# Kernel optimization log

Hardware: AMD Instinct MI355X
Metric: run time of the kernel (lower is better)

## Reference

```python
import jax, jax.numpy as jnp
import numpy as np

EMBED_DIM = 1024
NUM_HEADS = 16
HEAD_DIM = EMBED_DIM // NUM_HEADS

def setup_inputs() -> dict:
    key = jax.random.key(0)
    k1, k2, k3 = jax.random.split(key, 3)
    x = jax.random.normal(k1, (4, 2048, EMBED_DIM), dtype=jnp.float32)
    # Linear weights stored as [out, in] like torch; we apply x @ W.T
    W_qkv = jax.random.normal(k2, (3 * EMBED_DIM, EMBED_DIM), dtype=jnp.float32) * (EMBED_DIM ** -0.5)
    W_proj = jax.random.normal(k3, (EMBED_DIM, EMBED_DIM), dtype=jnp.float32) * (EMBED_DIM ** -0.5)
    return {"x": x, "W_qkv": W_qkv, "W_proj": W_proj}

def reference(x, W_qkv, W_proj):
    B, T, C = x.shape
    H, D = NUM_HEADS, HEAD_DIM
    qkv = x @ W_qkv.T                          # [B,T,3C]
    q, k, v = jnp.split(qkv, 3, axis=-1)
    q = q.reshape(B, T, H, D).transpose(0, 2, 1, 3)  # [B,H,T,D]
    k = k.reshape(B, T, H, D).transpose(0, 2, 1, 3)
    v = v.reshape(B, T, H, D).transpose(0, 2, 1, 3)
    scores = jnp.einsum('bhqd,bhkd->bhqk', q, k) / jnp.sqrt(jnp.asarray(D, x.dtype))
    causal = jnp.tril(jnp.ones((T, T), dtype=bool))
    scores = jnp.where(causal, scores, -jnp.inf)
    weights = jax.nn.softmax(scores, axis=-1)
    out = jnp.einsum('bhqk,bhkd->bhqd', weights, v)  # [B,H,T,D]
    out = out.transpose(0, 2, 1, 3).reshape(B, T, C)
    return out @ W_proj.T
```

## Files before the change

### kernel.cpp

```cpp
#include <hip/hip_runtime.h>

#define T_SEQ 2048
#define NB 4
#define NH 16
#define HD 64
#define CDIM 1024
#define MROWS (NB * T_SEQ)

typedef __attribute__((ext_vector_type(8))) short short8;
typedef __attribute__((ext_vector_type(4))) float floatx4;

static __device__ __forceinline__ unsigned short f2bf(float f) {
  union { float f; unsigned int i; } c; c.f = f;
  return (unsigned short)((c.i + 0x7FFFu + ((c.i >> 16) & 1u)) >> 16);
}
static __device__ __forceinline__ unsigned short f2bf_trunc(float f) {
  union { float f; unsigned int i; } c; c.f = f;
  return (unsigned short)(c.i >> 16);
}

static __device__ __forceinline__ void gl2lds16(const void* g, void* l) {
  __builtin_amdgcn_global_load_lds(
      (const __attribute__((address_space(1))) unsigned int*)g,
      (__attribute__((address_space(3))) unsigned int*)l, 16, 0, 0);
}

#define X4 (MROWS * CDIM / 4)
#define WQ4 (3 * CDIM * CDIM / 4)
#define WP4 (CDIM * CDIM / 4)
__global__ __launch_bounds__(256) void cast3_bf16(const float* __restrict__ x,
                                                  const float* __restrict__ wq,
                                                  const float* __restrict__ wp,
                                                  unsigned short* __restrict__ out) {
  const int i = blockIdx.x * 256 + threadIdx.x;
  const float* src; int off;
  if (i < X4) { src = x; off = i; }
  else if (i < X4 + WQ4) { src = wq; off = i - X4; }
  else { src = wp; off = i - X4 - WQ4; }
  const float4 v = ((const float4*)src)[off];
  ushort4 o;
  o.x = f2bf(v.x); o.y = f2bf(v.y); o.z = f2bf(v.z); o.w = f2bf(v.w);
  ((ushort4*)out)[i] = o;
}

#define Q_PRESCALE 0.18033688f

__global__ __launch_bounds__(256) void gemm_bf16_qkv(
    const unsigned short* __restrict__ A,
    const unsigned short* __restrict__ B,
    unsigned short* __restrict__ Oq,
    unsigned short* __restrict__ Ok,
    unsigned short* __restrict__ Ovt,
    const int K)
{
  __shared__ unsigned short As[2][128 * 32];
  __shared__ unsigned short Bs[2][128 * 32];
  const int tid = threadIdx.x;
  const int w = tid >> 6, l = tid & 63;
  const int quad = l >> 4, l15 = l & 15;
  const int m0 = blockIdx.y * 128, n0 = blockIdx.x * 128;
  const int wm = (w >> 1) * 64, wn = (w & 1) * 64;
  const int srow = l >> 2;
  const int scol = ((l & 3) ^ (srow & 3)) * 8;

  floatx4 acc[4][4];
#pragma unroll
  for (int mi = 0; mi < 4; ++mi)
#pragma unroll
    for (int ni = 0; ni < 4; ++ni) acc[mi][ni] = (floatx4){0.f, 0.f, 0.f, 0.f};

  const unsigned short* Ag = A + (size_t)(m0 + w * 32 + srow) * K + scol;
  const unsigned short* Bg = B + (size_t)(n0 + w * 32 + srow) * K + scol;
  const int d0 = (w * 32) * 32, d1 = (w * 32 + 16) * 32;
  const int sq = quad ^ (l15 & 3);

  gl2lds16(Ag, &As[0][d0]);
  gl2lds16(Ag + (size_t)16 * K, &As[0][d1]);
  gl2lds16(Bg, &Bs[0][d0]);
  gl2lds16(Bg + (size_t)16 * K, &Bs[0][d1]);

  for (int k0 = 0; k0 < K; k0 += 32) {
    const int cur = (k0 >> 5) & 1, nxt = 1 - cur;
    __syncthreads();
    if (k0 + 32 < K) {
      gl2lds16(Ag + k0 + 32, &As[nxt][d0]);
      gl2lds16(Ag + (size_t)16 * K + k0 + 32, &As[nxt][d1]);
      gl2lds16(Bg + k0 + 32, &Bs[nxt][d0]);
      gl2lds16(Bg + (size_t)16 * K + k0 + 32, &Bs[nxt][d1]);
    }
    short8 af[4], bfr[4];
#pragma unroll
    for (int mi = 0; mi < 4; ++mi)
      af[mi] = *(const short8*)&As[cur][(wm + mi * 16 + l15) * 32 + sq * 8];
#pragma unroll
    for (int ni = 0; ni < 4; ++ni)
      bfr[ni] = *(const short8*)&Bs[cur][(wn + ni * 16 + l15) * 32 + sq * 8];
#pragma unroll
    for (int mi = 0; mi < 4; ++mi)
#pragma unroll
      for (int ni = 0; ni < 4; ++ni)
        acc[mi][ni] = __builtin_amdgcn_mfma_f32_16x16x32_bf16(bfr[ni], af[mi], acc[mi][ni], 0, 0, 0);
  }

  const int which = n0 >> 10;
  if (which < 2) {
    unsigned short* dst = (which == 0) ? Oq : Ok;
    const float sc = (which == 0) ? Q_PRESCALE : 1.0f;
#pragma unroll
    for (int ni = 0; ni < 4; ++ni) {
      const int n = n0 + wn + ni * 16 + quad * 4;
      const int h = (n >> 6) & (NH - 1), d = n & (HD - 1);
#pragma unroll
      for (int mi = 0; mi < 4; ++mi) {
        const int m = m0 + wm + mi * 16 + l15;
        const int b = m >> 11, t = m & (T_SEQ - 1);
        ushort4 pk;
        pk.x = f2bf(acc[mi][ni][0] * sc); pk.y = f2bf(acc[mi][ni][1] * sc);
        pk.z = f2bf(acc[mi][ni][2] * sc); pk.w = f2bf(acc[mi][ni][3] * sc);
        *(ushort4*)(dst + (((size_t)(b * NH + h) * T_SEQ + t) << 6) + d) = pk;
      }
    }
  } else {
#pragma unroll
    for (int ni = 0; ni < 4; ++ni) {
      const int nb = n0 + wn + ni * 16 + quad * 4;
      const int h = (nb >> 6) & (NH - 1);
#pragma unroll
      for (int mi = 0; mi < 4; ++mi) {
        const int m = m0 + wm + mi * 16 + l15;
        const int b = m >> 11, t = m & (T_SEQ - 1);
#pragma unroll
        for (int r = 0; r < 4; ++r) {
          const int d = (nb + r) & (HD - 1);
          Ovt[((size_t)((b * NH + h) * HD + d) << 11) + t] = f2bf(acc[mi][ni][r]);
        }
      }
    }
  }
}

__global__ __launch_bounds__(256) void gemm_bf16_proj(
    const unsigned short* __restrict__ A,
    const unsigned short* __restrict__ B,
    float* __restrict__ O,
    const int N, const int K)
{
  __shared__ unsigned short As[2][128 * 32];
  __shared__ unsigned short Bs[2][128 * 32];
  const int tid = threadIdx.x;
  const int w = tid >> 6, l = tid & 63;
  const int quad = l >> 4, l15 = l & 15;
  const int m0 = blockIdx.y * 128, n0 = blockIdx.x * 128;
  const int wm = (w >> 1) * 64, wn = (w & 1) * 64;
  const int srow = l >> 2;
  const int scol = ((l & 3) ^ (srow & 3)) * 8;

  floatx4 acc[4][4];
#pragma unroll
  for (int mi = 0; mi < 4; ++mi)
#pragma unroll
    for (int ni = 0; ni < 4; ++ni) acc[mi][ni] = (floatx4){0.f, 0.f, 0.f, 0.f};

  const unsigned short* Ag = A + (size_t)(m0 + w * 32 + srow) * K + scol;
  const unsigned short* Bg = B + (size_t)(n0 + w * 32 + srow) * K + scol;
  const int d0 = (w * 32) * 32, d1 = (w * 32 + 16) * 32;
  const int sq = quad ^ (l15 & 3);

  gl2lds16(Ag, &As[0][d0]);
  gl2lds16(Ag + (size_t)16 * K, &As[0][d1]);
  gl2lds16(Bg, &Bs[0][d0]);
  gl2lds16(Bg + (size_t)16 * K, &Bs[0][d1]);

  for (int k0 = 0; k0 < K; k0 += 32) {
    const int cur = (k0 >> 5) & 1, nxt = 1 - cur;
    __syncthreads();
    if (k0 + 32 < K) {
      gl2lds16(Ag + k0 + 32, &As[nxt][d0]);
      gl2lds16(Ag + (size_t)16 * K + k0 + 32, &As[nxt][d1]);
      gl2lds16(Bg + k0 + 32, &Bs[nxt][d0]);
      gl2lds16(Bg + (size_t)16 * K + k0 + 32, &Bs[nxt][d1]);
    }
    short8 af[4], bfr[4];
#pragma unroll
    for (int mi = 0; mi < 4; ++mi)
      af[mi] = *(const short8*)&As[cur][(wm + mi * 16 + l15) * 32 + sq * 8];
#pragma unroll
    for (int ni = 0; ni < 4; ++ni)
      bfr[ni] = *(const short8*)&Bs[cur][(wn + ni * 16 + l15) * 32 + sq * 8];
#pragma unroll
    for (int mi = 0; mi < 4; ++mi)
#pragma unroll
      for (int ni = 0; ni < 4; ++ni)
        acc[mi][ni] = __builtin_amdgcn_mfma_f32_16x16x32_bf16(bfr[ni], af[mi], acc[mi][ni], 0, 0, 0);
  }

#pragma unroll
  for (int ni = 0; ni < 4; ++ni) {
    const int n = n0 + wn + ni * 16 + quad * 4;
#pragma unroll
    for (int mi = 0; mi < 4; ++mi) {
      const int m = m0 + wm + mi * 16 + l15;
      *(float4*)(O + (size_t)m * N + n) =
          make_float4(acc[mi][ni][0], acc[mi][ni][1], acc[mi][ni][2], acc[mi][ni][3]);
    }
  }
}

#define TK 64
#define PTP 72

__global__ __launch_bounds__(512) void attn_mfma(
    const unsigned short* __restrict__ Q,
    const unsigned short* __restrict__ K,
    const unsigned short* __restrict__ Vt,
    unsigned short* __restrict__ O)
{
  __shared__ unsigned short Ks[2][TK * HD];
  __shared__ unsigned short Vts[2][HD * TK];
  __shared__ unsigned short Pt[8][16 * PTP];
  const int tid = threadIdx.x;
  const int w = tid >> 6, l = tid & 63;
  const int quad = l >> 4, l15 = l & 15;
  const int drow = 8 * w + (l >> 3);
  const int dch = ((l & 7) ^ (l >> 3)) * 8;
  const int sw7 = l15 & 7;

  const int bh = blockIdx.x & 63;
  const int pp = blockIdx.x >> 6;
  const int b = bh >> 4, h = bh & 15;
  const size_t hoff = (size_t)bh * T_SEQ * HD;
  const unsigned short* Qh = Q + hoff;
  const unsigned short* Kdma = K + hoff + (size_t)drow * HD + dch;
  const unsigned short* Vdma = Vt + hoff + ((size_t)drow << 11) + dch;
  const int wb = w * 512;

  short8 ones;
#pragma unroll
  for (int j = 0; j < 8; ++j) ones[j] = (short)0x3F80;

#pragma unroll 1
  for (int ii = 0; ii < 2; ++ii) {
    const int qtile = ii ? pp : (15 - pp);
    const int qw = qtile * 128 + w * 16;

    short8 qf[2];
    {
      const int qrow = qw + l15;
      qf[0] = *(const short8*)(Qh + (size_t)qrow * HD + quad * 8);
      qf[1] = *(const short8*)(Qh + (size_t)qrow * HD + 32 + quad * 8);
    }

    floatx4 Of[4];
#pragma unroll
    for (int dc = 0; dc < 4; ++dc) Of[dc] = (floatx4){0.f, 0.f, 0.f, 0.f};
    floatx4 lacc = (floatx4){0.f, 0.f, 0.f, 0.f};

    const int nkt = 2 * qtile + 2;
    __syncthreads();
    gl2lds16(Kdma, &Ks[0][wb]);
    gl2lds16(Vdma, &Vts[0][wb]);

    for (int kt = 0; kt < nkt; ++kt) {
      const int kt0 = kt * TK;
      const int cur = kt & 1, nxt = 1 - cur;
      __syncthreads();
      if (kt + 1 < nkt) {
        gl2lds16(Kdma + (size_t)(kt0 + TK) * HD, &Ks[nxt][wb]);
        gl2lds16(Vdma + kt0 + TK, &Vts[nxt][wb]);
      }

      if (qw + 15 >= kt0) {
        floatx4 Sf[4];
#pragma unroll
        for (int cb = 0; cb < 4; ++cb) {
          Sf[cb] = (floatx4){0.f, 0.f, 0.f, 0.f};
          const int krow = cb * 16 + l15;
#pragma unroll
          for (int h2 = 0; h2 < 2; ++h2) {
            const int ch = (h2 * 4 + quad) ^ sw7;
            const short8 kf = *(const short8*)&Ks[cur][krow * 64 + ch * 8];
            Sf[cb] = __builtin_amdgcn_mfma_f32_16x16x32_bf16(kf, qf[h2], Sf[cb], 0, 0, 0);
          }
        }
        const bool full = (kt0 + 63 <= qw);
        const int q = qw + l15;
#pragma unroll
        for (int cb = 0; cb < 4; ++cb) {
          const int key0 = kt0 + cb * 16 + quad * 4;
          ushort4 pk;
          if (full) {
            pk.x = f2bf_trunc(exp2f(Sf[cb][0]));
            pk.y = f2bf_trunc(exp2f(Sf[cb][1]));
            pk.z = f2bf_trunc(exp2f(Sf[cb][2]));
            pk.w = f2bf_trunc(exp2f(Sf[cb][3]));
          } else {
            pk.x = (key0 + 0 > q) ? 0 : f2bf_trunc(exp2f(Sf[cb][0]));
            pk.y = (key0 + 1 > q) ? 0 : f2bf_trunc(exp2f(Sf[cb][1]));
            pk.z = (key0 + 2 > q) ? 0 : f2bf_trunc(exp2f(Sf[cb][2]));
            pk.w = (key0 + 3 > q) ? 0 : f2bf_trunc(exp2f(Sf[cb][3]));
          }
          *(ushort4*)&Pt[w][l15 * PTP + cb * 16 + quad * 4] = pk;
        }
#pragma unroll
        for (int kg = 0; kg < 2; ++kg) {
          const short8 ptf = *(const short8*)&Pt[w][l15 * PTP + kg * 32 + quad * 8];
          lacc = __builtin_amdgcn_mfma_f32_16x16x32_bf16(ones, ptf, lacc, 0, 0, 0);
#pragma unroll
          for (int dc = 0; dc < 4; ++dc) {
            const int vrow = dc * 16 + l15;
            const int ch = (kg * 4 + quad) ^ sw7;
            const short8 vf = *(const short8*)&Vts[cur][vrow * 64 + ch * 8];
            Of[dc] = __builtin_amdgcn_mfma_f32_16x16x32_bf16(vf, ptf, Of[dc], 0, 0, 0);
          }
        }
      }
    }

    const float inv = 1.f / lacc[0];
    const int q = qw + l15;
    unsigned short* orow = O + (size_t)(b * T_SEQ + q) * CDIM + h * HD + quad * 4;
#pragma unroll
    for (int dc = 0; dc < 4; ++dc) {
      ushort4 ov;
      ov.x = f2bf(Of[dc][0] * inv); ov.y = f2bf(Of[dc][1] * inv);
      ov.z = f2bf(Of[dc][2] * inv); ov.w = f2bf(Of[dc][3] * inv);
      *(ushort4*)(orow + dc * 16) = ov;
    }
  }
}

extern "C" void kernel_launch(void* const* d_in, const int* in_sizes, int n_in,
                              void* d_out, int out_size, void* d_ws, size_t ws_size,
                              hipStream_t stream) {
  const float* x     = (const float*)d_in[0];
  const float* Wqkv  = (const float*)d_in[1];
  const float* Wproj = (const float*)d_in[2];
  float* out = (float*)d_out;

  const size_t XSZ = (size_t)MROWS * CDIM;
  const size_t WQSZ = (size_t)3 * CDIM * CDIM;
  const size_t WPSZ = (size_t)CDIM * CDIM;
  unsigned short* xb  = (unsigned short*)d_ws;
  unsigned short* wqb = xb + XSZ;
  unsigned short* wpb = wqb + WQSZ;
  unsigned short* qbuf = wpb + WPSZ;
  unsigned short* kbuf = qbuf + XSZ;
  unsigned short* vtbuf = kbuf + XSZ;
  unsigned short* abuf = vtbuf + XSZ;

  cast3_bf16<<<(X4 + WQ4 + WP4) / 256, 256, 0, stream>>>(x, Wqkv, Wproj, xb);

  dim3 g1(3 * CDIM / 128, MROWS / 128);
  gemm_bf16_qkv<<<g1, 256, 0, stream>>>(xb, wqb, qbuf, kbuf, vtbuf, CDIM);

  attn_mfma<<<512, 512, 0, stream>>>(qbuf, kbuf, vtbuf, abuf);

  dim3 g3(CDIM / 128, MROWS / 128);
  gemm_bf16_proj<<<g3, 256, 0, stream>>>(abuf, wpb, out, CDIM, CDIM);
}
```

Before: 260.8 us.

## Rewrite QKV GEMM as 256x256 tile with staged quadrant pipelining

Replaces the 128x128 QKV projection GEMM with a 512-thread kernel that computes a 256x256 output tile, using K-steps of 64 and splitting each step into four MFMA quadrants. Global-to-LDS loads for the next halves are interleaved between quadrants with explicit barriers, vmcnt waits and s_setprio raised around the MFMA bursts. The aim is more data reuse per LDS load and better overlap of memory with compute. In exchange it uses much more LDS and registers per block and launches fewer blocks (384), which may hurt occupancy and load balance on the CU count.

```diff
diff --git a/kernel.cpp b/kernel.cpp
--- a/kernel.cpp
+++ b/kernel.cpp
@@ -45,7 +45,9 @@
 
 #define Q_PRESCALE 0.18033688f
 
-__global__ __launch_bounds__(256) void gemm_bf16_qkv(
+#define QNT (CDIM / 64)
+
+__global__ __launch_bounds__(512, 2) void gemm_bf16_qkv256(
     const unsigned short* __restrict__ A,
     const unsigned short* __restrict__ B,
     unsigned short* __restrict__ Oq,
@@ -53,54 +55,142 @@
     unsigned short* __restrict__ Ovt,
     const int K)
 {
-  __shared__ unsigned short As[2][128 * 32];
-  __shared__ unsigned short Bs[2][128 * 32];
+  __shared__ __align__(16) unsigned short As[2][2][128 * 64];
+  __shared__ __align__(16) unsigned short Bs[2][2][128 * 64];
   const int tid = threadIdx.x;
   const int w = tid >> 6, l = tid & 63;
   const int quad = l >> 4, l15 = l & 15;
-  const int m0 = blockIdx.y * 128, n0 = blockIdx.x * 128;
-  const int wm = (w >> 1) * 64, wn = (w & 1) * 64;
-  const int srow = l >> 2;
-  const int scol = ((l & 3) ^ (srow & 3)) * 8;
-
-  floatx4 acc[4][4];
-#pragma unroll
-  for (int mi = 0; mi < 4; ++mi)
+  const int wr = w >> 2, wc = w & 3;
+  const int m0 = blockIdx.y * 256, n0 = blockIdx.x * 256;
+
+  const int lrow = l >> 3;
+  const int lch = ((l & 7) ^ lrow) * 8;
+  const unsigned short* Ag = A + (size_t)(m0 + w * 16 + lrow) * K + lch;
+  const unsigned short* Bg = B + (size_t)(n0 + w * 16 + lrow) * K + lch;
+  const int ld0 = w * 1024, ld1 = w * 1024 + 512;
+  const size_t rsk = (size_t)8 * K;
+
+#define STAGE_A(buf, h, kof) do { \
+    gl2lds16(Ag + (size_t)(h) * 128 * K + (kof), &As[buf][h][ld0]); \
+    gl2lds16(Ag + (size_t)(h) * 128 * K + rsk + (kof), &As[buf][h][ld1]); } while (0)
+#define STAGE_B(buf, h, kof) do { \
+    gl2lds16(Bg + (size_t)(h) * 128 * K + (kof), &Bs[buf][h][ld0]); \
+    gl2lds16(Bg + (size_t)(h) * 128 * K + rsk + (kof), &Bs[buf][h][ld1]); } while (0)
+
+  const int sw7 = l15 & 7;
+  const int co0 = (quad ^ sw7) * 8;
+  const int co1 = co0 ^ 32;
+  const int fb = l15 * 64;
+  const unsigned short* Aw0 = &As[0][wr][0];
+  const unsigned short* Aw1 = &As[1][wr][0];
+  const unsigned short* Bw0 = &Bs[0][wc >> 1][(wc & 1) * 4096];
+  const unsigned short* Bw1 = &Bs[1][wc >> 1][(wc & 1) * 4096];
+
+  floatx4 acc[8][4];
+#pragma unroll
+  for (int mi = 0; mi < 8; ++mi)
 #pragma unroll
     for (int ni = 0; ni < 4; ++ni) acc[mi][ni] = (floatx4){0.f, 0.f, 0.f, 0.f};
 
-  const unsigned short* Ag = A + (size_t)(m0 + w * 32 + srow) * K + scol;
-  const unsigned short* Bg = B + (size_t)(n0 + w * 32 + srow) * K + scol;
-  const int d0 = (w * 32) * 32, d1 = (w * 32 + 16) * 32;
-  const int sq = quad ^ (l15 & 3);
-
-  gl2lds16(Ag, &As[0][d0]);
-  gl2lds16(Ag + (size_t)16 * K, &As[0][d1]);
-  gl2lds16(Bg, &Bs[0][d0]);
-  gl2lds16(Bg + (size_t)16 * K, &Bs[0][d1]);
-
-  for (int k0 = 0; k0 < K; k0 += 32) {
-    const int cur = (k0 >> 5) & 1, nxt = 1 - cur;
-    __syncthreads();
-    if (k0 + 32 < K) {
-      gl2lds16(Ag + k0 + 32, &As[nxt][d0]);
-      gl2lds16(Ag + (size_t)16 * K + k0 + 32, &As[nxt][d1]);
-      gl2lds16(Bg + k0 + 32, &Bs[nxt][d0]);
-      gl2lds16(Bg + (size_t)16 * K + k0 + 32, &Bs[nxt][d1]);
-    }
-    short8 af[4], bfr[4];
-#pragma unroll
-    for (int mi = 0; mi < 4; ++mi)
-      af[mi] = *(const short8*)&As[cur][(wm + mi * 16 + l15) * 32 + sq * 8];
-#pragma unroll
-    for (int ni = 0; ni < 4; ++ni)
-      bfr[ni] = *(const short8*)&Bs[cur][(wn + ni * 16 + l15) * 32 + sq * 8];
-#pragma unroll
-    for (int mi = 0; mi < 4; ++mi)
-#pragma unroll
-      for (int ni = 0; ni < 4; ++ni)
-        acc[mi][ni] = __builtin_amdgcn_mfma_f32_16x16x32_bf16(bfr[ni], af[mi], acc[mi][ni], 0, 0, 0);
+  STAGE_A(0, 0, 0); STAGE_A(0, 1, 0); STAGE_B(0, 0, 0); STAGE_B(0, 1, 0);
+  STAGE_B(1, 0, 64); STAGE_A(1, 0, 64);
+  asm volatile("s_waitcnt vmcnt(4)" ::: "memory");
+  __builtin_amdgcn_s_barrier();
+
+#pragma unroll 1
+  for (int j = 0; j < QNT; ++j) {
+    const int cur = j & 1, nxt = cur ^ 1;
+    const unsigned short* Ac = cur ? Aw1 : Aw0;
+    const unsigned short* Bc = cur ? Bw1 : Bw0;
+    const int kA = (j + 1) * 64, kC = (j + 2) * 64;
+    short8 aF[2][4], bL[2][2], bH[2][2];
+
+#pragma unroll
+    for (int mi = 0; mi < 4; ++mi) {
+      aF[0][mi] = *(const short8*)(Ac + mi * 1024 + fb + co0);
+      aF[1][mi] = *(const short8*)(Ac + mi * 1024 + fb + co1);
+    }
+#pragma unroll
+    for (int ni = 0; ni < 2; ++ni) {
+      bL[0][ni] = *(const short8*)(Bc + ni * 1024 + fb + co0);
+      bL[1][ni] = *(const short8*)(Bc + ni * 1024 + fb + co1);
+    }
+    if (j + 1 < QNT) STAGE_A(nxt, 1, kA);
+    __builtin_amdgcn_s_barrier();
+    asm volatile("s_waitcnt lgkmcnt(0)" ::: "memory");
+    __builtin_amdgcn_s_setprio(1);
+#pragma unroll
+    for (int ks = 0; ks < 2; ++ks)
+#pragma unroll
+      for (int mi = 0; mi < 4; ++mi)
+#pragma unroll
+        for (int ni = 0; ni < 2; ++ni)
+          acc[mi][ni] = __builtin_amdgcn_mfma_f32_16x16x32_bf16(
+              bL[ks][ni], aF[ks][mi], acc[mi][ni], 0, 0, 0);
+    __builtin_amdgcn_s_setprio(0);
+    __builtin_amdgcn_s_barrier();
+
+#pragma unroll
+    for (int ni = 0; ni < 2; ++ni) {
+      bH[0][ni] = *(const short8*)(Bc + (ni + 2) * 1024 + fb + co0);
+      bH[1][ni] = *(const short8*)(Bc + (ni + 2) * 1024 + fb + co1);
+    }
+    if (j + 1 < QNT) STAGE_B(nxt, 1, kA);
+    __builtin_amdgcn_s_barrier();
+    asm volatile("s_waitcnt lgkmcnt(0)" ::: "memory");
+    __builtin_amdgcn_s_setprio(1);
+#pragma unroll
+    for (int ks = 0; ks < 2; ++ks)
+#pragma unroll
+      for (int mi = 0; mi < 4; ++mi)
+#pragma unroll
+        for (int ni = 0; ni < 2; ++ni)
+          acc[mi][ni + 2] = __builtin_amdgcn_mfma_f32_16x16x32_bf16(
+              bH[ks][ni], aF[ks][mi], acc[mi][ni + 2], 0, 0, 0);
+    __builtin_amdgcn_s_setprio(0);
+    __builtin_amdgcn_s_barrier();
+
+#pragma unroll
+    for (int mi = 0; mi < 4; ++mi) {
+      aF[0][mi] = *(const short8*)(Ac + (mi + 4) * 1024 + fb + co0);
+      aF[1][mi] = *(const short8*)(Ac + (mi + 4) * 1024 + fb + co1);
+    }
+    if (j + 2 < QNT) STAGE_B(cur, 0, kC);
+    __builtin_amdgcn_s_barrier();
+    asm volatile("s_waitcnt lgkmcnt(0)" ::: "memory");
+    __builtin_amdgcn_s_setprio(1);
+#pragma unroll
+    for (int ks = 0; ks < 2; ++ks)
+#pragma unroll
+      for (int mi = 0; mi < 4; ++mi)
+#pragma unroll
+        for (int ni = 0; ni < 2; ++ni)
+          acc[mi + 4][ni] = __builtin_amdgcn_mfma_f32_16x16x32_bf16(
+              bL[ks][ni], aF[ks][mi], acc[mi + 4][ni], 0, 0, 0);
+    __builtin_amdgcn_s_setprio(0);
+    __builtin_amdgcn_s_barrier();
+
+    if (j + 2 < QNT) {
+      STAGE_A(cur, 0, kC);
+      asm volatile("s_waitcnt vmcnt(4)" ::: "memory");
+    } else {
+      asm volatile("s_waitcnt vmcnt(0)" ::: "memory");
+    }
+    __builtin_amdgcn_s_barrier();
+    __builtin_amdgcn_s_setprio(1);
+#pragma unroll
+    for (int ks = 0; ks < 2; ++ks)
+#pragma unroll
+      for (int mi = 0; mi < 4; ++mi)
+#pragma unroll
+        for (int ni = 0; ni < 2; ++ni)
+          acc[mi + 4][ni + 2] = __builtin_amdgcn_mfma_f32_16x16x32_bf16(
+              bH[ks][ni], aF[ks][mi], acc[mi + 4][ni + 2], 0, 0, 0);
+    __builtin_amdgcn_s_setprio(0);
+    __builtin_amdgcn_s_barrier();
   }
+#undef STAGE_A
+#undef STAGE_B
 
   const int which = n0 >> 10;
   if (which < 2) {
@@ -108,11 +198,11 @@
     const float sc = (which == 0) ? Q_PRESCALE : 1.0f;
 #pragma unroll
     for (int ni = 0; ni < 4; ++ni) {
-      const int n = n0 + wn + ni * 16 + quad * 4;
+      const int n = n0 + wc * 64 + ni * 16 + quad * 4;
       const int h = (n >> 6) & (NH - 1), d = n & (HD - 1);
 #pragma unroll
-      for (int mi = 0; mi < 4; ++mi) {
-        const int m = m0 + wm + mi * 16 + l15;
+      for (int mi = 0; mi < 8; ++mi) {
+        const int m = m0 + wr * 128 + mi * 16 + l15;
         const int b = m >> 11, t = m & (T_SEQ - 1);
         ushort4 pk;
         pk.x = f2bf(acc[mi][ni][0] * sc); pk.y = f2bf(acc[mi][ni][1] * sc);
@@ -123,11 +213,11 @@
   } else {
 #pragma unroll
     for (int ni = 0; ni < 4; ++ni) {
-      const int nb = n0 + wn + ni * 16 + quad * 4;
+      const int nb = n0 + wc * 64 + ni * 16 + quad * 4;
       const int h = (nb >> 6) & (NH - 1);
 #pragma unroll
-      for (int mi = 0; mi < 4; ++mi) {
-        const int m = m0 + wm + mi * 16 + l15;
+      for (int mi = 0; mi < 8; ++mi) {
+        const int m = m0 + wr * 128 + mi * 16 + l15;
         const int b = m >> 11, t = m & (T_SEQ - 1);
 #pragma unroll
         for (int r = 0; r < 4; ++r) {
@@ -350,8 +440,8 @@
 
   cast3_bf16<<<(X4 + WQ4 + WP4) / 256, 256, 0, stream>>>(x, Wqkv, Wproj, xb);
 
-  dim3 g1(3 * CDIM / 128, MROWS / 128);
-  gemm_bf16_qkv<<<g1, 256, 0, stream>>>(xb, wqb, qbuf, kbuf, vtbuf, CDIM);
+  dim3 g1(3 * CDIM / 256, MROWS / 256);
+  gemm_bf16_qkv256<<<g1, 512, 0, stream>>>(xb, wqb, qbuf, kbuf, vtbuf, CDIM);
 
   attn_mfma<<<512, 512, 0, stream>>>(qbuf, kbuf, vtbuf, abuf);
 
```

Measured after the change: 254.2 us. -2.5%, faster.

## Rewrite QKV GEMM with 256x192 tiles, BK=64 and split-phase pipelined staging

Applied to the files above, without the earlier changes.

Replaces the 128x128x32 QKV projection GEMM with a 512-thread kernel that computes a 256x192 output tile at K-step 64. It uses a wider XOR swizzle, splits the next-tile global-to-LDS loads across two compute phases with explicit vmcnt waits and barriers, and raises wave priority around the MFMA bursts. The goal is more data reuse per LDS byte, fewer barriers per FLOP, and better overlap of memory with compute. In exchange it uses much more LDS (about 112 KB) and more accumulator registers per thread, which limits occupancy. It also relies on hand-tuned waitcnt counts that must match the issued loads exactly.

```diff
diff --git a/kernel.cpp b/kernel.cpp
--- a/kernel.cpp
+++ b/kernel.cpp
@@ -45,7 +45,9 @@
 
 #define Q_PRESCALE 0.18033688f
 
-__global__ __launch_bounds__(256) void gemm_bf16_qkv(
+#define QNT (CDIM / 64)
+
+__global__ __launch_bounds__(512, 2) void gemm_bf16_qkv192(
     const unsigned short* __restrict__ A,
     const unsigned short* __restrict__ B,
     unsigned short* __restrict__ Oq,
@@ -53,86 +55,132 @@
     unsigned short* __restrict__ Ovt,
     const int K)
 {
-  __shared__ unsigned short As[2][128 * 32];
-  __shared__ unsigned short Bs[2][128 * 32];
+  __shared__ __align__(16) unsigned short As[2][256 * 64];
+  __shared__ __align__(16) unsigned short Bs[2][192 * 64];
   const int tid = threadIdx.x;
   const int w = tid >> 6, l = tid & 63;
   const int quad = l >> 4, l15 = l & 15;
-  const int m0 = blockIdx.y * 128, n0 = blockIdx.x * 128;
-  const int wm = (w >> 1) * 64, wn = (w & 1) * 64;
-  const int srow = l >> 2;
-  const int scol = ((l & 3) ^ (srow & 3)) * 8;
-
-  floatx4 acc[4][4];
-#pragma unroll
-  for (int mi = 0; mi < 4; ++mi)
-#pragma unroll
-    for (int ni = 0; ni < 4; ++ni) acc[mi][ni] = (floatx4){0.f, 0.f, 0.f, 0.f};
-
-  const unsigned short* Ag = A + (size_t)(m0 + w * 32 + srow) * K + scol;
-  const unsigned short* Bg = B + (size_t)(n0 + w * 32 + srow) * K + scol;
-  const int d0 = (w * 32) * 32, d1 = (w * 32 + 16) * 32;
-  const int sq = quad ^ (l15 & 3);
-
-  gl2lds16(Ag, &As[0][d0]);
-  gl2lds16(Ag + (size_t)16 * K, &As[0][d1]);
-  gl2lds16(Bg, &Bs[0][d0]);
-  gl2lds16(Bg + (size_t)16 * K, &Bs[0][d1]);
-
-  for (int k0 = 0; k0 < K; k0 += 32) {
-    const int cur = (k0 >> 5) & 1, nxt = 1 - cur;
-    __syncthreads();
-    if (k0 + 32 < K) {
-      gl2lds16(Ag + k0 + 32, &As[nxt][d0]);
-      gl2lds16(Ag + (size_t)16 * K + k0 + 32, &As[nxt][d1]);
-      gl2lds16(Bg + k0 + 32, &Bs[nxt][d0]);
-      gl2lds16(Bg + (size_t)16 * K + k0 + 32, &Bs[nxt][d1]);
-    }
-    short8 af[4], bfr[4];
-#pragma unroll
-    for (int mi = 0; mi < 4; ++mi)
-      af[mi] = *(const short8*)&As[cur][(wm + mi * 16 + l15) * 32 + sq * 8];
-#pragma unroll
-    for (int ni = 0; ni < 4; ++ni)
-      bfr[ni] = *(const short8*)&Bs[cur][(wn + ni * 16 + l15) * 32 + sq * 8];
-#pragma unroll
-    for (int mi = 0; mi < 4; ++mi)
-#pragma unroll
-      for (int ni = 0; ni < 4; ++ni)
-        acc[mi][ni] = __builtin_amdgcn_mfma_f32_16x16x32_bf16(bfr[ni], af[mi], acc[mi][ni], 0, 0, 0);
+  const int wr = w >> 2, wc = w & 3;
+  const int m0 = blockIdx.y * 256, n0 = blockIdx.x * 192;
+
+  const int st_row = tid >> 3;
+  const int st_sch = ((tid & 7) ^ (st_row & 7)) * 8;
+  const unsigned short* Ast = A + (size_t)(m0 + st_row) * K + st_sch;
+  const unsigned short* Bst = B + (size_t)(n0 + st_row) * K + st_sch;
+  const int dst8 = tid * 8;
+
+#define STG_A(buf, c, kof) gl2lds16(Ast + (size_t)(c) * 64 * K + (kof), \
+                                    &As[buf][(c) * 4096 + dst8])
+#define STG_B(buf, c, kof) gl2lds16(Bst + (size_t)(c) * 64 * K + (kof), \
+                                    &Bs[buf][(c) * 4096 + dst8])
+
+  const int sw7 = l15 & 7;
+  const int co0 = (quad ^ sw7) * 8;
+  const int co1 = co0 ^ 32;
+  const unsigned short* Aw0 = &As[0][wr * 8192 + l15 * 64];
+  const unsigned short* Aw1 = &As[1][wr * 8192 + l15 * 64];
+  const unsigned short* Bw0 = &Bs[0][wc * 3072 + l15 * 64];
+  const unsigned short* Bw1 = &Bs[1][wc * 3072 + l15 * 64];
+
+  floatx4 acc[8][3];
+#pragma unroll
+  for (int mi = 0; mi < 8; ++mi)
+#pragma unroll
+    for (int ni = 0; ni < 3; ++ni) acc[mi][ni] = (floatx4){0.f, 0.f, 0.f, 0.f};
+
+  STG_A(0, 0, 0); STG_A(0, 1, 0); STG_A(0, 2, 0); STG_A(0, 3, 0);
+  STG_B(0, 0, 0); STG_B(0, 1, 0); STG_B(0, 2, 0);
+  asm volatile("s_waitcnt vmcnt(0)" ::: "memory");
+  __builtin_amdgcn_s_barrier();
+
+#pragma unroll 1
+  for (int j = 0; j < QNT; ++j) {
+    const int cur = j & 1, nxt = cur ^ 1;
+    const unsigned short* Ac = cur ? Aw1 : Aw0;
+    const unsigned short* Bc = cur ? Bw1 : Bw0;
+    const int k1 = (j + 1) * 64;
+    short8 aF[2][4], bF[2][3];
+
+    if (j + 1 < QNT) {
+      STG_A(nxt, 0, k1); STG_A(nxt, 2, k1);
+      STG_B(nxt, 0, k1); STG_B(nxt, 1, k1); STG_B(nxt, 2, k1);
+    }
+#pragma unroll
+    for (int mi = 0; mi < 4; ++mi) {
+      aF[0][mi] = *(const short8*)(Ac + mi * 1024 + co0);
+      aF[1][mi] = *(const short8*)(Ac + mi * 1024 + co1);
+    }
+#pragma unroll
+    for (int ni = 0; ni < 3; ++ni) {
+      bF[0][ni] = *(const short8*)(Bc + ni * 1024 + co0);
+      bF[1][ni] = *(const short8*)(Bc + ni * 1024 + co1);
+    }
+    __builtin_amdgcn_s_barrier();
+    asm volatile("s_waitcnt lgkmcnt(0)" ::: "memory");
+    __builtin_amdgcn_s_setprio(1);
+#pragma unroll
+    for (int ks = 0; ks < 2; ++ks)
+#pragma unroll
+      for (int mi = 0; mi < 4; ++mi)
+#pragma unroll
+        for (int ni = 0; ni < 3; ++ni)
+          acc[mi][ni] = __builtin_amdgcn_mfma_f32_16x16x32_bf16(
+              bF[ks][ni], aF[ks][mi], acc[mi][ni], 0, 0, 0);
+    __builtin_amdgcn_s_setprio(0);
+    if (j + 1 < QNT) asm volatile("s_waitcnt vmcnt(5)" ::: "memory");
+    else             asm volatile("s_waitcnt vmcnt(0)" ::: "memory");
+    __builtin_amdgcn_s_barrier();
+
+    if (j + 1 < QNT) { STG_A(nxt, 1, k1); STG_A(nxt, 3, k1); }
+#pragma unroll
+    for (int mi = 0; mi < 4; ++mi) {
+      aF[0][mi] = *(const short8*)(Ac + (mi + 4) * 1024 + co0);
+      aF[1][mi] = *(const short8*)(Ac + (mi + 4) * 1024 + co1);
+    }
+    __builtin_amdgcn_s_barrier();
+    asm volatile("s_waitcnt lgkmcnt(0)" ::: "memory");
+    __builtin_amdgcn_s_setprio(1);
+#pragma unroll
+    for (int ks = 0; ks < 2; ++ks)
+#pragma unroll
+      for (int mi = 0; mi < 4; ++mi)
+#pragma unroll
+        for (int ni = 0; ni < 3; ++ni)
+          acc[mi + 4][ni] = __builtin_amdgcn_mfma_f32_16x16x32_bf16(
+              bF[ks][ni], aF[ks][mi], acc[mi + 4][ni], 0, 0, 0);
+    __builtin_amdgcn_s_setprio(0);
+    if (j + 1 < QNT) asm volatile("s_waitcnt vmcnt(2)" ::: "memory");
+    __builtin_amdgcn_s_barrier();
   }
-
-  const int which = n0 >> 10;
-  if (which < 2) {
-    unsigned short* dst = (which == 0) ? Oq : Ok;
-    const float sc = (which == 0) ? Q_PRESCALE : 1.0f;
-#pragma unroll
-    for (int ni = 0; ni < 4; ++ni) {
-      const int n = n0 + wn + ni * 16 + quad * 4;
-      const int h = (n >> 6) & (NH - 1), d = n & (HD - 1);
-#pragma unroll
-      for (int mi = 0; mi < 4; ++mi) {
-        const int m = m0 + wm + mi * 16 + l15;
-        const int b = m >> 11, t = m & (T_SEQ - 1);
+#undef STG_A
+#undef STG_B
+
+#pragma unroll
+  for (int ni = 0; ni < 3; ++ni) {
+    const int n = n0 + wc * 48 + ni * 16 + quad * 4;
+    const int which = n >> 10;
+    const int h = (n >> 6) & (NH - 1), d = n & (HD - 1);
+#pragma unroll
+    for (int mi = 0; mi < 8; ++mi) {
+      const int m = m0 + wr * 128 + mi * 16 + l15;
+      const int b = m >> 11, t = m & (T_SEQ - 1);
+      if (which == 0) {
         ushort4 pk;
-        pk.x = f2bf(acc[mi][ni][0] * sc); pk.y = f2bf(acc[mi][ni][1] * sc);
-        pk.z = f2bf(acc[mi][ni][2] * sc); pk.w = f2bf(acc[mi][ni][3] * sc);
-        *(ushort4*)(dst + (((size_t)(b * NH + h) * T_SEQ + t) << 6) + d) = pk;
-      }
-    }
-  } else {
-#pragma unroll
-    for (int ni = 0; ni < 4; ++ni) {
-      const int nb = n0 + wn + ni * 16 + quad * 4;
-      const int h = (nb >> 6) & (NH - 1);
-#pragma unroll
-      for (int mi = 0; mi < 4; ++mi) {
-        const int m = m0 + wm + mi * 16 + l15;
-        const int b = m >> 11, t = m & (T_SEQ - 1);
+        pk.x = f2bf(acc[mi][ni][0] * Q_PRESCALE);
+        pk.y = f2bf(acc[mi][ni][1] * Q_PRESCALE);
+        pk.z = f2bf(acc[mi][ni][2] * Q_PRESCALE);
+        pk.w = f2bf(acc[mi][ni][3] * Q_PRESCALE);
+        *(ushort4*)(Oq + (((size_t)(b * NH + h) * T_SEQ + t) << 6) + d) = pk;
+      } else if (which == 1) {
+        ushort4 pk;
+        pk.x = f2bf(acc[mi][ni][0]); pk.y = f2bf(acc[mi][ni][1]);
+        pk.z = f2bf(acc[mi][ni][2]); pk.w = f2bf(acc[mi][ni][3]);
+        *(ushort4*)(Ok + (((size_t)(b * NH + h) * T_SEQ + t) << 6) + d) = pk;
+      } else {
 #pragma unroll
         for (int r = 0; r < 4; ++r) {
-          const int d = (nb + r) & (HD - 1);
-          Ovt[((size_t)((b * NH + h) * HD + d) << 11) + t] = f2bf(acc[mi][ni][r]);
+          const int dv = (n + r) & (HD - 1);
+          Ovt[((size_t)((b * NH + h) * HD + dv) << 11) + t] = f2bf(acc[mi][ni][r]);
         }
       }
     }
@@ -350,8 +398,8 @@
 
   cast3_bf16<<<(X4 + WQ4 + WP4) / 256, 256, 0, stream>>>(x, Wqkv, Wproj, xb);
 
-  dim3 g1(3 * CDIM / 128, MROWS / 128);
-  gemm_bf16_qkv<<<g1, 256, 0, stream>>>(xb, wqb, qbuf, kbuf, vtbuf, CDIM);
+  dim3 g1(3 * CDIM / 192, MROWS / 256);
+  gemm_bf16_qkv192<<<g1, 512, 0, stream>>>(xb, wqb, qbuf, kbuf, vtbuf, CDIM);
 
   attn_mfma<<<512, 512, 0, stream>>>(qbuf, kbuf, vtbuf, abuf);
 
```

After: 266.9 us. 1.02x slower.
